# Kernel optimization log

Measured on AMD Instinct MI355X. Metric: run time of the kernel, lower is better.

## Reference

```python
import jax, jax.numpy as jnp
import numpy as np

M, N, D = 8192, 8192, 64

def setup_inputs() -> dict:
    key = jax.random.key(0)
    k1, k2 = jax.random.split(key)
    X = jax.random.normal(k1, (M, D), dtype=jnp.float32)
    Y = jax.random.normal(k2, (N, D), dtype=jnp.float32)
    gamma_param = jnp.asarray(1.0, dtype=jnp.float32)  # learnable scalar (rbf branch)
    return {"X": X, "Y": Y, "gamma_param": gamma_param}

def reference(X, Y, gamma_param):
    # RBF kernel: exp(-gamma * ||x_i - y_j||^2), (m, n)
    x_sq = jnp.sum(X * X, axis=-1)          # (m,)
    y_sq = jnp.sum(Y * Y, axis=-1)          # (n,)
    xy = jnp.einsum("md,nd->mn", X, Y)      # (m, n)
    sq_norm = x_sq[:, None] + y_sq[None, :] - 2.0 * xy
    sq_norm = jnp.maximum(sq_norm, 0.0)     # numerical clamp
    return jnp.exp(-gamma_param * sq_norm)
```

## Files before the change

kernel.cpp:

```cpp
#include <hip/hip_runtime.h>

#define MTOT 8192
#define NTOT 8192
#define DD   64
#define SPLIT (MTOT * DD)

typedef __bf16 bf16x8 __attribute__((ext_vector_type(8)));
typedef float  f32x16 __attribute__((ext_vector_type(16)));
typedef unsigned short u16;
typedef unsigned short u16x4 __attribute__((ext_vector_type(4)));
typedef unsigned short u16x8 __attribute__((ext_vector_type(8)));

__device__ __forceinline__ u16 bf16_rne(float v) {
    unsigned int u = __float_as_uint(v);
    u = u + 0x7FFFu + ((u >> 16) & 1u);
    return (u16)(u >> 16);
}
__device__ __forceinline__ float bf16_to_f32(u16 h) {
    return __uint_as_float(((unsigned int)h) << 16);
}

#define MFMA(a, b, c) __builtin_amdgcn_mfma_f32_32x32x16_bf16((a), (b), (c), 0, 0, 0)

__device__ __forceinline__ void load_lds_16B(const u16* g, u16* lds_uniform) {
    __builtin_amdgcn_global_load_lds(
        (const __attribute__((address_space(1))) unsigned int*)g,
        (__attribute__((address_space(3))) unsigned int*)lds_uniform,
        16, 0, 0);
}

__global__ __launch_bounds__(256)
void rbf_pre_kernel(const float* __restrict__ X, const float* __restrict__ Y,
                    u16* __restrict__ XhiF, u16* __restrict__ XloF,
                    u16* __restrict__ YhiF, u16* __restrict__ YloF,
                    float* __restrict__ xqs, float* __restrict__ yqs)
{
    const int gid = blockIdx.x * 256 + threadIdx.x;
    const int mat = gid >> 15;
    const int r4  = gid & 32767;
    const int row = r4 >> 2;
    const int q   = r4 & 3;
    const float* src = mat ? Y : X;
    u16* hi  = mat ? YhiF : XhiF;
    u16* lo  = mat ? YloF : XloF;
    float* nrm = mat ? yqs : xqs;

    const long rbase = (long)row * DD + q * 16;
    float s = 0.f;
    u16x8 h0, h1, l0, l1;
    #pragma unroll
    for (int c = 0; c < 4; ++c) {
        const float4 v = *reinterpret_cast<const float4*>(src + rbase + c * 4);
        const float vv[4] = {v.x, v.y, v.z, v.w};
        #pragma unroll
        for (int e = 0; e < 4; ++e) {
            const int idx = c * 4 + e;
            const float x = vv[e];
            s = fmaf(x, x, s);
            const u16 hh = bf16_rne(x);
            const u16 ll = bf16_rne(x - bf16_to_f32(hh));
            if (idx < 8) { h0[idx] = hh; l0[idx] = ll; }
            else         { h1[idx - 8] = hh; l1[idx - 8] = ll; }
        }
    }
    s += __shfl_xor(s, 1);
    s += __shfl_xor(s, 2);
    if (q == 0) nrm[row] = s;

    const int tt = row >> 5, lr = row & 31;
    const long fbase = (long)(tt * 4 + q) * 512;
    *reinterpret_cast<u16x8*>(hi + fbase + lr * 8)        = h0;
    *reinterpret_cast<u16x8*>(hi + fbase + (32 + lr) * 8) = h1;
    *reinterpret_cast<u16x8*>(lo + fbase + lr * 8)        = l0;
    *reinterpret_cast<u16x8*>(lo + fbase + (32 + lr) * 8) = l1;
}

__global__ __launch_bounds__(256, 2)
void rbf_fused_kernel(const u16* __restrict__ XhiF, const u16* __restrict__ XloF,
                      const u16* __restrict__ YhiF, const u16* __restrict__ YloF,
                      const float* __restrict__ xqs, const float* __restrict__ yqs,
                      const float* __restrict__ gamma_p,
                      float* __restrict__ out)
{
    __shared__ __align__(16) u16 S[4][8192];

    const int t = threadIdx.x;
    const int w = t >> 6;
    const int l = t & 63;
    const int loff = l * 8;

    const int bid = blockIdx.x;
    const int swz = ((bid & 7) << 9) | (bid >> 3);
    const int bm = swz >> 6;
    const int bn = swz & 63;
    const long row0 = (long)bm * 128;
    const long col0 = (long)bn * 128;

    {
        const u16* gsrc;
        if      (w == 0) gsrc = XhiF + (long)bm * 8192;
        else if (w == 1) gsrc = XloF + (long)bm * 8192;
        else if (w == 2) gsrc = YhiF + (long)bn * 8192;
        else             gsrc = YloF + (long)bn * 8192;
        #pragma unroll
        for (int c = 0; c < 16; ++c)
            load_lds_16B(gsrc + c * 512 + loff, &S[w][c * 512]);
    }

    const float g  = gamma_p[0];
    const float g2 = 2.0f * g;
    const int  mt0 = (w >> 1) * 2;
    const int  nt0 = (w & 1) * 2;
    const int l5x4 = (l >> 5) * 4;
    const int  ln  = l & 31;

    float xv[2][16];
    #pragma unroll
    for (int ii = 0; ii < 2; ++ii)
        #pragma unroll
        for (int q4 = 0; q4 < 4; ++q4) {
            const float4 x4 = *reinterpret_cast<const float4*>(
                xqs + row0 + (mt0 + ii) * 32 + 8 * q4 + l5x4);
            xv[ii][q4 * 4 + 0] = x4.x; xv[ii][q4 * 4 + 1] = x4.y;
            xv[ii][q4 * 4 + 2] = x4.z; xv[ii][q4 * 4 + 3] = x4.w;
        }
    float cy[2];
    #pragma unroll
    for (int jj = 0; jj < 2; ++jj)
        cy[jj] = -g * yqs[col0 + (nt0 + jj) * 32 + ln];

    __syncthreads();

    bf16x8 aH[2][4], aL[2][4];
    #pragma unroll
    for (int ii = 0; ii < 2; ++ii)
        #pragma unroll
        for (int ks = 0; ks < 4; ++ks) {
            aH[ii][ks] = *reinterpret_cast<const bf16x8*>(&S[0][((mt0 + ii) * 4 + ks) * 512 + loff]);
            aL[ii][ks] = *reinterpret_cast<const bf16x8*>(&S[1][((mt0 + ii) * 4 + ks) * 512 + loff]);
        }

    #pragma unroll
    for (int qq = 0; qq < 4; ++qq) {
        const int ii = qq & 1;
        const int jj = qq >> 1;

        bf16x8 bH[4], bL[4];
        #pragma unroll
        for (int ks = 0; ks < 4; ++ks) {
            bH[ks] = *reinterpret_cast<const bf16x8*>(&S[2][((nt0 + jj) * 4 + ks) * 512 + loff]);
            bL[ks] = *reinterpret_cast<const bf16x8*>(&S[3][((nt0 + jj) * 4 + ks) * 512 + loff]);
        }

        f32x16 acc;
        #pragma unroll
        for (int r = 0; r < 16; ++r) acc[r] = 0.f;
        #pragma unroll
        for (int ks = 0; ks < 4; ++ks) {
            acc = MFMA(aH[ii][ks], bH[ks], acc);
            acc = MFMA(aH[ii][ks], bL[ks], acc);
            acc = MFMA(aL[ii][ks], bH[ks], acc);
        }

        const int  mt  = mt0 + ii;
        const long gc  = col0 + (nt0 + jj) * 32 + ln;
        float* const orow = out + (row0 + mt * 32) * (long)NTOT + gc;
        const float cyj = cy[jj];
        #pragma unroll
        for (int r = 0; r < 16; ++r) {
            float arg = fmaf(g2, acc[r], fmaf(-g, xv[ii][r], cyj));
            arg = fminf(arg, 0.f);
            const int rr = (r & 3) + 8 * (r >> 2) + l5x4;
            __builtin_nontemporal_store(__expf(arg), orow + rr * (long)NTOT);
        }
    }
}

__global__ __launch_bounds__(256, 2)
void rbf_fallback_kernel(const float* __restrict__ X,
                         const float* __restrict__ Y,
                         const float* __restrict__ gamma_p,
                         float* __restrict__ out)
{
    __shared__ unsigned short XfH[4][4][64][8];
    __shared__ unsigned short XfL[4][4][64][8];
    __shared__ unsigned short YfH[4][4][64][8];
    __shared__ unsigned short YfL[4][4][64][8];
    __shared__ float xq[128];
    __shared__ float yq[128];

    const int t = threadIdx.x;
    const long row0 = (long)blockIdx.y * 128;
    const long col0 = (long)blockIdx.x * 128;

    {
        const int k0   = (t & 15) * 4;
        const int ks   = k0 >> 4;
        const int l32  = ((k0 >> 3) & 1) << 5;
        const int slot = k0 & 4;
        #pragma unroll
        for (int i = 0; i < 8; ++i) {
            const int row  = (t >> 4) + i * 16;
            const int mt   = row >> 5;
            const int lane = (row & 31) | l32;
            const float4 vx = *reinterpret_cast<const float4*>(X + (row0 + row) * DD + k0);
            const float4 vy = *reinterpret_cast<const float4*>(Y + (col0 + row) * DD + k0);
            float xv[4] = {vx.x, vx.y, vx.z, vx.w};
            float yv[4] = {vy.x, vy.y, vy.z, vy.w};
            u16x4 xh, xl, yh, yl;
            #pragma unroll
            for (int e = 0; e < 4; ++e) {
                const u16 hx = bf16_rne(xv[e]);
                xh[e] = hx; xl[e] = bf16_rne(xv[e] - bf16_to_f32(hx));
                const u16 hy = bf16_rne(yv[e]);
                yh[e] = hy; yl[e] = bf16_rne(yv[e] - bf16_to_f32(hy));
            }
            *reinterpret_cast<u16x4*>(&XfH[mt][ks][lane][slot]) = xh;
            *reinterpret_cast<u16x4*>(&XfL[mt][ks][lane][slot]) = xl;
            *reinterpret_cast<u16x4*>(&YfH[mt][ks][lane][slot]) = yh;
            *reinterpret_cast<u16x4*>(&YfL[mt][ks][lane][slot]) = yl;
        }
    }
    {
        const int r = t & 127;
        const float* p2 = (t < 128) ? (X + (row0 + r) * DD) : (Y + (col0 + r) * DD);
        float s0 = 0.f, s1 = 0.f, s2 = 0.f, s3 = 0.f;
        #pragma unroll
        for (int c = 0; c < 16; ++c) {
            const float4 v = reinterpret_cast<const float4*>(p2)[c];
            s0 = fmaf(v.x, v.x, s0); s1 = fmaf(v.y, v.y, s1);
            s2 = fmaf(v.z, v.z, s2); s3 = fmaf(v.w, v.w, s3);
        }
        const float s = (s0 + s1) + (s2 + s3);
        if (t < 128) xq[r] = s; else yq[r] = s;
    }
    __syncthreads();

    const int w = t >> 6;
    const int l = t & 63;
    const int mt0 = (w >> 1) * 2;
    const int nt0 = (w & 1) * 2;

    bf16x8 aH[2][4], aL[2][4];
    #pragma unroll
    for (int i = 0; i < 2; ++i)
        #pragma unroll
        for (int ks = 0; ks < 4; ++ks) {
            aH[i][ks] = *reinterpret_cast<const bf16x8*>(&XfH[mt0 + i][ks][l][0]);
            aL[i][ks] = *reinterpret_cast<const bf16x8*>(&XfL[mt0 + i][ks][l][0]);
        }

    f32x16 acc[2][2];
    #pragma unroll
    for (int i = 0; i < 2; ++i)
        #pragma unroll
        for (int j = 0; j < 2; ++j)
            #pragma unroll
            for (int r = 0; r < 16; ++r) acc[i][j][r] = 0.f;

    #pragma unroll
    for (int ks = 0; ks < 4; ++ks) {
        const bf16x8 b0h = *reinterpret_cast<const bf16x8*>(&YfH[nt0 + 0][ks][l][0]);
        const bf16x8 b1h = *reinterpret_cast<const bf16x8*>(&YfH[nt0 + 1][ks][l][0]);
        const bf16x8 b0l = *reinterpret_cast<const bf16x8*>(&YfL[nt0 + 0][ks][l][0]);
        const bf16x8 b1l = *reinterpret_cast<const bf16x8*>(&YfL[nt0 + 1][ks][l][0]);
        acc[0][0] = MFMA(aH[0][ks], b0h, acc[0][0]);
        acc[0][1] = MFMA(aH[0][ks], b1h, acc[0][1]);
        acc[1][0] = MFMA(aH[1][ks], b0h, acc[1][0]);
        acc[1][1] = MFMA(aH[1][ks], b1h, acc[1][1]);
        acc[0][0] = MFMA(aH[0][ks], b0l, acc[0][0]);
        acc[0][1] = MFMA(aH[0][ks], b1l, acc[0][1]);
        acc[1][0] = MFMA(aH[1][ks], b0l, acc[1][0]);
        acc[1][1] = MFMA(aH[1][ks], b1l, acc[1][1]);
        acc[0][0] = MFMA(aL[0][ks], b0h, acc[0][0]);
        acc[0][1] = MFMA(aL[0][ks], b1h, acc[0][1]);
        acc[1][0] = MFMA(aL[1][ks], b0h, acc[1][0]);
        acc[1][1] = MFMA(aL[1][ks], b1h, acc[1][1]);
    }

    const float g = gamma_p[0];
    const int l5x4 = (l >> 5) * 4;
    const int ln = l & 31;
    #pragma unroll
    for (int i = 0; i < 2; ++i) {
        const int mt = mt0 + i;
        float xv[16];
        #pragma unroll
        for (int r = 0; r < 16; ++r)
            xv[r] = xq[mt * 32 + (r & 3) + 8 * (r >> 2) + l5x4];
        #pragma unroll
        for (int j = 0; j < 2; ++j) {
            const int nt = nt0 + j;
            const float yv = yq[nt * 32 + ln];
            const long gr = row0 + mt * 32;
            const long gc = col0 + nt * 32 + ln;
            #pragma unroll
            for (int r = 0; r < 16; ++r) {
                float s = fmaf(-2.f, acc[i][j][r], xv[r] + yv);
                s = fmaxf(s, 0.f);
                const long rr = gr + (r & 3) + 8 * (r >> 2) + l5x4;
                out[rr * NTOT + gc] = __expf(-g * s);
            }
        }
    }
}

extern "C" void kernel_launch(void* const* d_in, const int* in_sizes, int n_in,
                              void* d_out, int out_size, void* d_ws, size_t ws_size,
                              hipStream_t stream) {
    (void)in_sizes; (void)n_in; (void)out_size;
    const float* X = (const float*)d_in[0];
    const float* Y = (const float*)d_in[1];
    const float* gamma_p = (const float*)d_in[2];
    float* out = (float*)d_out;

    const size_t need = 4 * (size_t)SPLIT * sizeof(u16) + (MTOT + NTOT) * sizeof(float);

    if (ws_size >= need) {
        u16* XhiF = (u16*)d_ws;
        u16* XloF = XhiF + SPLIT;
        u16* YhiF = XloF + SPLIT;
        u16* YloF = YhiF + SPLIT;
        float* xqs = (float*)(YloF + SPLIT);
        float* yqs = xqs + MTOT;
        rbf_pre_kernel<<<256, 256, 0, stream>>>(X, Y, XhiF, XloF, YhiF, YloF, xqs, yqs);
        rbf_fused_kernel<<<4096, 256, 0, stream>>>(XhiF, XloF, YhiF, YloF, xqs, yqs, gamma_p, out);
    } else {
        dim3 grid(NTOT / 128, MTOT / 128);
        rbf_fallback_kernel<<<grid, 256, 0, stream>>>(X, Y, gamma_p, out);
    }
}
```

Baseline: 57.44 us.

## Give each wave a full 32-row slab and store full 128-column rows

Each wave now owns a 32x128 row slab instead of a 2x2 set of 32x32 tiles. It keeps four accumulators live and writes each output row as four 32-wide segments, so a wavefront's stores cover contiguous 512-byte row spans. The direct global-to-LDS async load is replaced by ordinary global loads followed by LDS stores. This trades more live accumulator registers, which may hurt occupancy, and loses the async LDS load path in exchange for better store coalescing.

```diff
diff --git a/kernel.cpp b/kernel.cpp
--- a/kernel.cpp
+++ b/kernel.cpp
@@ -21,13 +21,6 @@
 }
 
 #define MFMA(a, b, c) __builtin_amdgcn_mfma_f32_32x32x16_bf16((a), (b), (c), 0, 0, 0)
-
-__device__ __forceinline__ void load_lds_16B(const u16* g, u16* lds_uniform) {
-    __builtin_amdgcn_global_load_lds(
-        (const __attribute__((address_space(1))) unsigned int*)g,
-        (__attribute__((address_space(3))) unsigned int*)lds_uniform,
-        16, 0, 0);
-}
 
 __global__ __launch_bounds__(256)
 void rbf_pre_kernel(const float* __restrict__ X, const float* __restrict__ Y,
@@ -76,11 +69,11 @@
 }
 
 __global__ __launch_bounds__(256, 2)
-void rbf_fused_kernel(const u16* __restrict__ XhiF, const u16* __restrict__ XloF,
-                      const u16* __restrict__ YhiF, const u16* __restrict__ YloF,
-                      const float* __restrict__ xqs, const float* __restrict__ yqs,
-                      const float* __restrict__ gamma_p,
-                      float* __restrict__ out)
+void rbf_rowslab_kernel(const u16* __restrict__ XhiF, const u16* __restrict__ XloF,
+                        const u16* __restrict__ YhiF, const u16* __restrict__ YloF,
+                        const float* __restrict__ xqs, const float* __restrict__ yqs,
+                        const float* __restrict__ gamma_p,
+                        float* __restrict__ out)
 {
     __shared__ __align__(16) u16 S[4][8192];
 
@@ -102,77 +95,81 @@
         else if (w == 1) gsrc = XloF + (long)bm * 8192;
         else if (w == 2) gsrc = YhiF + (long)bn * 8192;
         else             gsrc = YloF + (long)bn * 8192;
-        #pragma unroll
-        for (int c = 0; c < 16; ++c)
-            load_lds_16B(gsrc + c * 512 + loff, &S[w][c * 512]);
+        u16* const ldst = &S[w][0];
+        #pragma unroll
+        for (int c = 0; c < 16; ++c) {
+            const int off = c * 512 + loff;
+            *reinterpret_cast<int4*>(ldst + off) = *reinterpret_cast<const int4*>(gsrc + off);
+        }
     }
 
     const float g  = gamma_p[0];
     const float g2 = 2.0f * g;
-    const int  mt0 = (w >> 1) * 2;
-    const int  nt0 = (w & 1) * 2;
     const int l5x4 = (l >> 5) * 4;
     const int  ln  = l & 31;
 
-    float xv[2][16];
-    #pragma unroll
-    for (int ii = 0; ii < 2; ++ii)
-        #pragma unroll
-        for (int q4 = 0; q4 < 4; ++q4) {
-            const float4 x4 = *reinterpret_cast<const float4*>(
-                xqs + row0 + (mt0 + ii) * 32 + 8 * q4 + l5x4);
-            xv[ii][q4 * 4 + 0] = x4.x; xv[ii][q4 * 4 + 1] = x4.y;
-            xv[ii][q4 * 4 + 2] = x4.z; xv[ii][q4 * 4 + 3] = x4.w;
-        }
-    float cy[2];
-    #pragma unroll
-    for (int jj = 0; jj < 2; ++jj)
-        cy[jj] = -g * yqs[col0 + (nt0 + jj) * 32 + ln];
+    float xv[16];
+    #pragma unroll
+    for (int q4 = 0; q4 < 4; ++q4) {
+        const float4 x4 = *reinterpret_cast<const float4*>(
+            xqs + row0 + w * 32 + 8 * q4 + l5x4);
+        xv[q4 * 4 + 0] = x4.x; xv[q4 * 4 + 1] = x4.y;
+        xv[q4 * 4 + 2] = x4.z; xv[q4 * 4 + 3] = x4.w;
+    }
+    const float cy0 = -g * yqs[col0 +  0 + ln];
+    const float cy1 = -g * yqs[col0 + 32 + ln];
+    const float cy2 = -g * yqs[col0 + 64 + ln];
+    const float cy3 = -g * yqs[col0 + 96 + ln];
 
     __syncthreads();
 
-    bf16x8 aH[2][4], aL[2][4];
-    #pragma unroll
-    for (int ii = 0; ii < 2; ++ii)
-        #pragma unroll
-        for (int ks = 0; ks < 4; ++ks) {
-            aH[ii][ks] = *reinterpret_cast<const bf16x8*>(&S[0][((mt0 + ii) * 4 + ks) * 512 + loff]);
-            aL[ii][ks] = *reinterpret_cast<const bf16x8*>(&S[1][((mt0 + ii) * 4 + ks) * 512 + loff]);
-        }
-
-    #pragma unroll
-    for (int qq = 0; qq < 4; ++qq) {
-        const int ii = qq & 1;
-        const int jj = qq >> 1;
-
-        bf16x8 bH[4], bL[4];
-        #pragma unroll
-        for (int ks = 0; ks < 4; ++ks) {
-            bH[ks] = *reinterpret_cast<const bf16x8*>(&S[2][((nt0 + jj) * 4 + ks) * 512 + loff]);
-            bL[ks] = *reinterpret_cast<const bf16x8*>(&S[3][((nt0 + jj) * 4 + ks) * 512 + loff]);
-        }
-
-        f32x16 acc;
-        #pragma unroll
-        for (int r = 0; r < 16; ++r) acc[r] = 0.f;
-        #pragma unroll
-        for (int ks = 0; ks < 4; ++ks) {
-            acc = MFMA(aH[ii][ks], bH[ks], acc);
-            acc = MFMA(aH[ii][ks], bL[ks], acc);
-            acc = MFMA(aL[ii][ks], bH[ks], acc);
-        }
-
-        const int  mt  = mt0 + ii;
-        const long gc  = col0 + (nt0 + jj) * 32 + ln;
-        float* const orow = out + (row0 + mt * 32) * (long)NTOT + gc;
-        const float cyj = cy[jj];
-        #pragma unroll
-        for (int r = 0; r < 16; ++r) {
-            float arg = fmaf(g2, acc[r], fmaf(-g, xv[ii][r], cyj));
-            arg = fminf(arg, 0.f);
-            const int rr = (r & 3) + 8 * (r >> 2) + l5x4;
-            __builtin_nontemporal_store(__expf(arg), orow + rr * (long)NTOT);
-        }
+    bf16x8 aH[4], aL[4];
+    #pragma unroll
+    for (int ks = 0; ks < 4; ++ks) {
+        aH[ks] = *reinterpret_cast<const bf16x8*>(&S[0][(w * 4 + ks) * 512 + loff]);
+        aL[ks] = *reinterpret_cast<const bf16x8*>(&S[1][(w * 4 + ks) * 512 + loff]);
+    }
+
+    f32x16 q0, q1, q2, q3;
+    #pragma unroll
+    for (int r = 0; r < 16; ++r) { q0[r] = 0.f; q1[r] = 0.f; q2[r] = 0.f; q3[r] = 0.f; }
+
+#define QUAD(ACC, JJ)                                                                   \
+    {                                                                                   \
+        bf16x8 bh[4], bl[4];                                                            \
+        _Pragma("unroll")                                                               \
+        for (int ks = 0; ks < 4; ++ks) {                                                \
+            bh[ks] = *reinterpret_cast<const bf16x8*>(&S[2][((JJ) * 4 + ks) * 512 + loff]); \
+            bl[ks] = *reinterpret_cast<const bf16x8*>(&S[3][((JJ) * 4 + ks) * 512 + loff]); \
+        }                                                                               \
+        _Pragma("unroll")                                                               \
+        for (int ks = 0; ks < 4; ++ks) {                                                \
+            ACC = MFMA(aH[ks], bh[ks], ACC);                                            \
+            ACC = MFMA(aH[ks], bl[ks], ACC);                                            \
+            ACC = MFMA(aL[ks], bh[ks], ACC);                                            \
+        }                                                                               \
+    }
+
+    QUAD(q0, 0)
+    QUAD(q1, 1)
+    QUAD(q2, 2)
+    QUAD(q3, 3)
+#undef QUAD
+
+    float* const obase = out + (row0 + w * 32) * (long)NTOT + col0 + ln;
+    #pragma unroll
+    for (int r = 0; r < 16; ++r) {
+        const int rr = (r & 3) + 8 * (r >> 2) + l5x4;
+        float* const orow = obase + rr * (long)NTOT;
+        const float nx = -g * xv[r];
+        const float a0 = fminf(fmaf(g2, q0[r], nx + cy0), 0.f);
+        const float a1 = fminf(fmaf(g2, q1[r], nx + cy1), 0.f);
+        const float a2 = fminf(fmaf(g2, q2[r], nx + cy2), 0.f);
+        const float a3 = fminf(fmaf(g2, q3[r], nx + cy3), 0.f);
+        __builtin_nontemporal_store(__expf(a0), orow);
+        __builtin_nontemporal_store(__expf(a1), orow + 32);
+        __builtin_nontemporal_store(__expf(a2), orow + 64);
+        __builtin_nontemporal_store(__expf(a3), orow + 96);
     }
 }
 
@@ -324,7 +321,7 @@
         float* xqs = (float*)(YloF + SPLIT);
         float* yqs = xqs + MTOT;
         rbf_pre_kernel<<<256, 256, 0, stream>>>(X, Y, XhiF, XloF, YhiF, YloF, xqs, yqs);
-        rbf_fused_kernel<<<4096, 256, 0, stream>>>(XhiF, XloF, YhiF, YloF, xqs, yqs, gamma_p, out);
+        rbf_rowslab_kernel<<<4096, 256, 0, stream>>>(XhiF, XloF, YhiF, YloF, xqs, yqs, gamma_p, out);
     } else {
         dim3 grid(NTOT / 128, MTOT / 128);
         rbf_fallback_kernel<<<grid, 256, 0, stream>>>(X, Y, gamma_p, out);
```

Result: slower. 61.74 us (+7.5%).
